# Performance work log

Measured on AMD Instinct MI355X. Metric: run time of the kernel, lower is better.

The kernel has to match this reference:

```python
import jax, jax.numpy as jnp
import numpy as np

B, FIN, FOUT, H, W = 16, 16, 16, 384, 384
LAT, NMIX = 512, 8


def setup_inputs() -> dict:
    key = jax.random.key(0)
    ks = jax.random.split(key, 6)
    x = jax.random.normal(ks[0], (B, FIN, H, W), dtype=jnp.float32)
    lat = jax.random.normal(ks[1], (B, LAT), dtype=jnp.float32)
    # kernel_mix: [n_mix, fout, fin] (kernel_size=1 dims squeezed); xavier-normal-ish scale
    kernel_mix = jax.random.normal(ks[2], (NMIX, FOUT, FIN), dtype=jnp.float32) * np.sqrt(2.0 / (FIN + FOUT))
    bias_mix = jax.random.normal(ks[3], (NMIX, FOUT), dtype=jnp.float32) * np.sqrt(2.0 / (NMIX + FOUT))
    # dyna_mix Linear(lat_size, n_mix)
    w_dyn = jax.random.normal(ks[4], (NMIX, LAT), dtype=jnp.float32) * np.sqrt(1.0 / LAT)
    b_dyn = jax.random.normal(ks[5], (NMIX,), dtype=jnp.float32) * 0.01
    return {"x": x, "lat": lat, "kernel_mix": kernel_mix, "bias_mix": bias_mix,
            "w_dyn": w_dyn, "b_dyn": b_dyn}


def reference(x, lat, kernel_mix, bias_mix, w_dyn, b_dyn):
    # mixing coefficients per sample: [B, n_mix]
    mix = lat @ w_dyn.T + b_dyn
    # per-sample dynamic 1x1 kernel: [B, fout, fin]
    kernel = jnp.einsum('bm,moi->boi', mix, kernel_mix)
    # per-sample dynamic bias: [B, fout]
    bias = jnp.einsum('bm,mo->bo', mix, bias_mix)
    # grouped conv with batch*groups groups on 1x1 kernel == per-sample matmul over channels
    out = jnp.einsum('bihw,boi->bohw', x, kernel) + bias[:, :, None, None]
    return out
```

## Files before the change

### kernel.cpp

```cpp
#include <hip/hip_runtime.h>

#define BB   16
#define FIN  16
#define FOUT 16
#define HH   384
#define WW   384
#define LAT  512
#define NMIX 8
#define HW   (HH * WW)
#define HW4  (HW / 4)

__global__ __launch_bounds__(256)
void mix_prep_kernel(const float* __restrict__ lat,
                     const float* __restrict__ kernel_mix,
                     const float* __restrict__ bias_mix,
                     const float* __restrict__ w_dyn,
                     const float* __restrict__ b_dyn,
                     float* __restrict__ kbuf,
                     float* __restrict__ bbuf) {
    __shared__ float mix_s[BB][NMIX];
    const int t = threadIdx.x;

    if (t < BB * NMIX) {
        const int b = t / NMIX, m = t % NMIX;
        const float4* lv = (const float4*)(lat + (size_t)b * LAT);
        const float4* wv = (const float4*)(w_dyn + (size_t)m * LAT);
        float acc = 0.f;
#pragma unroll 8
        for (int j = 0; j < LAT / 4; ++j) {
            float4 a = lv[j], w = wv[j];
            acc += a.x * w.x + a.y * w.y + a.z * w.z + a.w * w.w;
        }
        mix_s[b][m] = acc + b_dyn[m];
    }
    __syncthreads();

    const int b = t / FOUT, o = t % FOUT;
    float kacc[FIN];
#pragma unroll
    for (int i = 0; i < FIN; ++i) kacc[i] = 0.f;
    float bacc = 0.f;
#pragma unroll
    for (int m = 0; m < NMIX; ++m) {
        const float c = mix_s[b][m];
        bacc += c * bias_mix[m * FOUT + o];
#pragma unroll
        for (int i = 0; i < FIN; ++i)
            kacc[i] += c * kernel_mix[(m * FOUT + o) * FIN + i];
    }
    bbuf[b * FOUT + o] = bacc;
#pragma unroll
    for (int i = 0; i < FIN; ++i)
        kbuf[(b * FOUT + o) * FIN + i] = kacc[i];
}

__global__ __launch_bounds__(256)
void mixconv_main(const float* __restrict__ x,
                  const float* __restrict__ kbuf,
                  const float* __restrict__ bbuf,
                  float* __restrict__ out) {
    const int b = blockIdx.y;
    const int p = blockIdx.x * 256 + threadIdx.x;

    const float4* xv = (const float4*)(x + (size_t)b * FIN * HW) + p;
    float4*       ov = (float4*)(out + (size_t)b * FOUT * HW) + p;

    float4 xi[FIN];
#pragma unroll
    for (int i = 0; i < FIN; ++i) xi[i] = xv[(size_t)i * HW4];

    const float* k  = kbuf + b * FOUT * FIN;
    const float* bv = bbuf + b * FOUT;

#pragma unroll
    for (int o = 0; o < FOUT; ++o) {
        const float bo = bv[o];
        float4 acc;
        acc.x = bo; acc.y = bo; acc.z = bo; acc.w = bo;
#pragma unroll
        for (int i = 0; i < FIN; ++i) {
            const float kv = k[o * FIN + i];
            acc.x += kv * xi[i].x;
            acc.y += kv * xi[i].y;
            acc.z += kv * xi[i].z;
            acc.w += kv * xi[i].w;
        }
        ov[(size_t)o * HW4] = acc;
    }
}

extern "C" void kernel_launch(void* const* d_in, const int* in_sizes, int n_in,
                              void* d_out, int out_size, void* d_ws, size_t ws_size,
                              hipStream_t stream) {
    const float* x          = (const float*)d_in[0];
    const float* lat        = (const float*)d_in[1];
    const float* kernel_mix = (const float*)d_in[2];
    const float* bias_mix   = (const float*)d_in[3];
    const float* w_dyn      = (const float*)d_in[4];
    const float* b_dyn      = (const float*)d_in[5];
    float* out = (float*)d_out;

    float* kbuf = (float*)d_ws;
    float* bbuf = kbuf + BB * FOUT * FIN;

    mix_prep_kernel<<<dim3(1), dim3(256), 0, stream>>>(
        lat, kernel_mix, bias_mix, w_dyn, b_dyn, kbuf, bbuf);

    dim3 grid(HW4 / 256, BB);
    mixconv_main<<<grid, dim3(256), 0, stream>>>(x, kbuf, bbuf, out);
}
```

Before: 288.4 us.

## Fuse mix-coefficient prep into main conv kernel with nontemporal streaming

Removes the separate single-block prep kernel and computes the per-sample mixing coefficients, dynamic kernel and bias inside each block of the main kernel, staged in shared memory. The per-block reduction is parallelized across all 256 threads. X loads and output stores use nontemporal builtins to avoid cache pollution. This eliminates a launch and the serial dependency, at the cost of redundant prep work and extra barriers in every block.

New measurement: 260.4 us. 9.7% less time.

```diff
diff --git a/kernel.cpp b/kernel.cpp
--- a/kernel.cpp
+++ b/kernel.cpp
@@ -10,82 +10,88 @@
 #define HW   (HH * WW)
 #define HW4  (HW / 4)
 
+typedef float f32x4 __attribute__((ext_vector_type(4)));
+
 __global__ __launch_bounds__(256)
-void mix_prep_kernel(const float* __restrict__ lat,
-                     const float* __restrict__ kernel_mix,
-                     const float* __restrict__ bias_mix,
-                     const float* __restrict__ w_dyn,
-                     const float* __restrict__ b_dyn,
-                     float* __restrict__ kbuf,
-                     float* __restrict__ bbuf) {
-    __shared__ float mix_s[BB][NMIX];
+void mixconv_fused(const float* __restrict__ x,
+                   const float* __restrict__ lat,
+                   const float* __restrict__ kernel_mix,
+                   const float* __restrict__ bias_mix,
+                   const float* __restrict__ w_dyn,
+                   const float* __restrict__ b_dyn,
+                   float* __restrict__ out) {
+    __shared__ float part[NMIX][32];
+    __shared__ float mix_s[NMIX];
+    __shared__ float ksh[FOUT][FIN];
+    __shared__ float bsh[FOUT];
+
     const int t = threadIdx.x;
+    const int b = blockIdx.y;
 
-    if (t < BB * NMIX) {
-        const int b = t / NMIX, m = t % NMIX;
-        const float4* lv = (const float4*)(lat + (size_t)b * LAT);
-        const float4* wv = (const float4*)(w_dyn + (size_t)m * LAT);
+    {
+        const int m = t & (NMIX - 1);
+        const int c = t >> 3;
+        const f32x4* lv = (const f32x4*)(lat + (size_t)b * LAT + c * 16);
+        const f32x4* wv = (const f32x4*)(w_dyn + (size_t)m * LAT + c * 16);
         float acc = 0.f;
-#pragma unroll 8
-        for (int j = 0; j < LAT / 4; ++j) {
-            float4 a = lv[j], w = wv[j];
+#pragma unroll
+        for (int j = 0; j < 4; ++j) {
+            f32x4 a = lv[j], w = wv[j];
             acc += a.x * w.x + a.y * w.y + a.z * w.z + a.w * w.w;
         }
-        mix_s[b][m] = acc + b_dyn[m];
+        part[m][c] = acc;
+    }
+    __syncthreads();
+    if (t < NMIX) {
+        float s = 0.f;
+#pragma unroll
+        for (int c = 0; c < 32; ++c) s += part[t][c];
+        mix_s[t] = s + b_dyn[t];
     }
     __syncthreads();
 
-    const int b = t / FOUT, o = t % FOUT;
-    float kacc[FIN];
+    {
+        float kacc = 0.f;
 #pragma unroll
-    for (int i = 0; i < FIN; ++i) kacc[i] = 0.f;
-    float bacc = 0.f;
+        for (int m = 0; m < NMIX; ++m)
+            kacc += mix_s[m] * kernel_mix[m * FOUT * FIN + t];
+        ((float*)ksh)[t] = kacc;
+        if (t < FOUT) {
+            float bacc = 0.f;
 #pragma unroll
-    for (int m = 0; m < NMIX; ++m) {
-        const float c = mix_s[b][m];
-        bacc += c * bias_mix[m * FOUT + o];
-#pragma unroll
-        for (int i = 0; i < FIN; ++i)
-            kacc[i] += c * kernel_mix[(m * FOUT + o) * FIN + i];
+            for (int m = 0; m < NMIX; ++m)
+                bacc += mix_s[m] * bias_mix[m * FOUT + t];
+            bsh[t] = bacc;
+        }
     }
-    bbuf[b * FOUT + o] = bacc;
+    __syncthreads();
+
+    const int p = blockIdx.x * 256 + t;
+    const f32x4* xv = (const f32x4*)(x + (size_t)b * FIN * HW) + p;
+    f32x4*       ov = (f32x4*)(out + (size_t)b * FOUT * HW) + p;
+
+    f32x4 xi[FIN];
 #pragma unroll
     for (int i = 0; i < FIN; ++i)
-        kbuf[(b * FOUT + o) * FIN + i] = kacc[i];
-}
-
-__global__ __launch_bounds__(256)
-void mixconv_main(const float* __restrict__ x,
-                  const float* __restrict__ kbuf,
-                  const float* __restrict__ bbuf,
-                  float* __restrict__ out) {
-    const int b = blockIdx.y;
-    const int p = blockIdx.x * 256 + threadIdx.x;
-
-    const float4* xv = (const float4*)(x + (size_t)b * FIN * HW) + p;
-    float4*       ov = (float4*)(out + (size_t)b * FOUT * HW) + p;
-
-    float4 xi[FIN];
-#pragma unroll
-    for (int i = 0; i < FIN; ++i) xi[i] = xv[(size_t)i * HW4];
-
-    const float* k  = kbuf + b * FOUT * FIN;
-    const float* bv = bbuf + b * FOUT;
+        xi[i] = __builtin_nontemporal_load(xv + (size_t)i * HW4);
 
 #pragma unroll
     for (int o = 0; o < FOUT; ++o) {
-        const float bo = bv[o];
-        float4 acc;
-        acc.x = bo; acc.y = bo; acc.z = bo; acc.w = bo;
-#pragma unroll
-        for (int i = 0; i < FIN; ++i) {
-            const float kv = k[o * FIN + i];
-            acc.x += kv * xi[i].x;
-            acc.y += kv * xi[i].y;
-            acc.z += kv * xi[i].z;
-            acc.w += kv * xi[i].w;
-        }
-        ov[(size_t)o * HW4] = acc;
+        const f32x4 k0 = *(const f32x4*)&ksh[o][0];
+        const f32x4 k1 = *(const f32x4*)&ksh[o][4];
+        const f32x4 k2 = *(const f32x4*)&ksh[o][8];
+        const f32x4 k3 = *(const f32x4*)&ksh[o][12];
+        const float bo = bsh[o];
+        f32x4 acc = {bo, bo, bo, bo};
+        acc += k0.x * xi[0];  acc += k0.y * xi[1];
+        acc += k0.z * xi[2];  acc += k0.w * xi[3];
+        acc += k1.x * xi[4];  acc += k1.y * xi[5];
+        acc += k1.z * xi[6];  acc += k1.w * xi[7];
+        acc += k2.x * xi[8];  acc += k2.y * xi[9];
+        acc += k2.z * xi[10]; acc += k2.w * xi[11];
+        acc += k3.x * xi[12]; acc += k3.y * xi[13];
+        acc += k3.z * xi[14]; acc += k3.w * xi[15];
+        __builtin_nontemporal_store(acc, ov + (size_t)o * HW4);
     }
 }
 
@@ -100,12 +106,7 @@
     const float* b_dyn      = (const float*)d_in[5];
     float* out = (float*)d_out;
 
-    float* kbuf = (float*)d_ws;
-    float* bbuf = kbuf + BB * FOUT * FIN;
-
-    mix_prep_kernel<<<dim3(1), dim3(256), 0, stream>>>(
-        lat, kernel_mix, bias_mix, w_dyn, b_dyn, kbuf, bbuf);
-
     dim3 grid(HW4 / 256, BB);
-    mixconv_main<<<grid, dim3(256), 0, stream>>>(x, kbuf, bbuf, out);
+    mixconv_fused<<<grid, dim3(256), 0, stream>>>(
+        x, lat, kernel_mix, bias_mix, w_dyn, b_dyn, out);
 }
```
